# Kernel tuning notes

Hardware: AMD Instinct MI355X
Metric: run time of the kernel (lower is better)

## Reference

```python
import jax, jax.numpy as jnp
import numpy as np

SIG = [1, 1, 1, 1, -1]  # Cl(4,1)
NVEC = 5
GA = 1 << NVEC  # 32


def _build_gp_table():
    # Cayley table for the geometric product on blades indexed by bitmask.
    G = np.zeros((GA, GA, GA), np.float32)
    for a in range(GA):
        for b in range(GA):
            s = 0
            t = a >> 1
            while t:
                s += bin(t & b).count('1')
                t >>= 1
            sign = -1.0 if (s & 1) else 1.0
            common = a & b
            for i in range(NVEC):
                if (common >> i) & 1:
                    sign *= SIG[i]
            G[a, b, a ^ b] = sign
    return G

GP_TABLE = jnp.asarray(_build_gp_table())


def geometric_product(x, y):
    return jnp.einsum('...i,...j,ijk->...k', x, y, GP_TABLE)


def manifold_norm(x):
    # normalize each multivector onto the unit sphere in R^32
    return x / (jnp.linalg.norm(x, axis=-1, keepdims=True) + 1e-6)


def versor_linear(x, W, b):
    # channel mixing shared across multivector components: x [..., in, ga]
    return jnp.einsum('...ig,oi->...og', x, W) + b


def layer_norm2d(x, w, b):
    # LayerNorm over last two dims [D, ga] jointly
    mu = jnp.mean(x, axis=(-2, -1), keepdims=True)
    var = jnp.var(x, axis=(-2, -1), keepdims=True)
    return (x - mu) / jnp.sqrt(var + 1e-5) * w + b


def attention(x, Wq, bq, Wk, bk, Wv, bv, Wo, bo, n_heads):
    B, S, D, G = x.shape
    dh = D // n_heads
    q = versor_linear(x, Wq, bq).reshape(B, S, n_heads, dh, G)
    k = versor_linear(x, Wk, bk).reshape(B, S, n_heads, dh, G)
    v = versor_linear(x, Wv, bv).reshape(B, S, n_heads, dh, G)
    scale = 1.0 / np.sqrt(dh * G).astype(np.float32)
    scores = jnp.einsum('bshdg,bthdg->bhst', q, k) * scale
    probs = jax.nn.softmax(scores, axis=-1)
    o = jnp.einsum('bhst,bthdg->bshdg', probs, v).reshape(B, S, D, G)
    return versor_linear(o, Wo, bo)


N_HEADS = 8


def forward(x, Wq, bq, Wk, bk, Wv, bv, Wo, bo, ln1_w, ln1_b, ln2_w, ln2_b,
            gamma1, gamma2, W1, b1, W2, b2, Wr, br, Wc, bc):
    L = Wq.shape[0]
    for l in range(L):
        h = attention(layer_norm2d(x, ln1_w[l], ln1_b[l]),
                      Wq[l], bq[l], Wk[l], bk[l], Wv[l], bv[l], Wo[l], bo[l], N_HEADS)
        x = manifold_norm(x + gamma1[l] * h)
        m = versor_linear(layer_norm2d(x, ln2_w[l], ln2_b[l]), W1[l], b1[l])
        m = versor_linear(jnp.tanh(m), W2[l], b2[l])
        x = manifold_norm(x + gamma2[l] * m)
    # RecursiveRotorAccumulator: log(S)-step inclusive scan of rotors
    delta = versor_linear(x, Wr, br)
    rot = 0.5 * delta
    rot = rot.at[..., 0].add(1.0)
    rot = manifold_norm(rot)
    S = x.shape[1]
    step = 1
    while step < S:
        left = rot[:, :-step]
        right = rot[:, step:]
        comb = manifold_norm(geometric_product(right, left))
        rot = jnp.concatenate([rot[:, :step], comb], axis=1)
        step *= 2
    pooled = rot[:, -1]  # [B, D, ga]
    logits = pooled.reshape(pooled.shape[0], -1) @ Wc.T + bc
    return logits


def setup_inputs() -> dict:
    key = jax.random.key(0)
    B, S, D, G, L, NC = 8, 256, 64, GA, 4, 1000
    E = 4 * D  # expansion hidden
    ks = jax.random.split(key, 16)
    sd = 0.02
    inp = {
        'x': jax.random.normal(ks[0], (B, S, D, G), jnp.float32),
        'Wq': jax.random.normal(ks[1], (L, D, D), jnp.float32) * sd,
        'bq': jnp.zeros((L, D, G), jnp.float32),
        'Wk': jax.random.normal(ks[2], (L, D, D), jnp.float32) * sd,
        'bk': jnp.zeros((L, D, G), jnp.float32),
        'Wv': jax.random.normal(ks[3], (L, D, D), jnp.float32) * sd,
        'bv': jnp.zeros((L, D, G), jnp.float32),
        'Wo': jax.random.normal(ks[4], (L, D, D), jnp.float32) * sd,
        'bo': jnp.zeros((L, D, G), jnp.float32),
        'ln1_w': jnp.ones((L, D, G), jnp.float32),
        'ln1_b': jnp.zeros((L, D, G), jnp.float32),
        'ln2_w': jnp.ones((L, D, G), jnp.float32),
        'ln2_b': jnp.zeros((L, D, G), jnp.float32),
        'gamma1': 1e-5 * jnp.ones((L, D, G), jnp.float32),
        'gamma2': 1e-5 * jnp.ones((L, D, G), jnp.float32),
        'W1': jax.random.normal(ks[5], (L, E, D), jnp.float32) * sd,
        'b1': jnp.zeros((L, E, G), jnp.float32),
        'W2': jax.random.normal(ks[6], (L, D, E), jnp.float32) * sd,
        'b2': jnp.zeros((L, D, G), jnp.float32),
        'Wr': jax.random.normal(ks[7], (D, D), jnp.float32) * sd,
        'br': jnp.zeros((D, G), jnp.float32),
        'Wc': jax.random.normal(ks[8], (NC, D * G), jnp.float32) * sd,
        'bc': jnp.zeros((NC,), jnp.float32),
    }
    return inp


def reference(x, Wq, bq, Wk, bk, Wv, bv, Wo, bo, ln1_w, ln1_b, ln2_w, ln2_b,
              gamma1, gamma2, W1, b1, W2, b2, Wr, br, Wc, bc):
    return forward(x, Wq, bq, Wk, bk, Wv, bv, Wo, bo, ln1_w, ln1_b, ln2_w, ln2_b,
                   gamma1, gamma2, W1, b1, W2, b2, Wr, br, Wc, bc)
```

## Files before the change

### kernel.cpp

```cpp
#include <hip/hip_runtime.h>
#include <hip/hip_bf16.h>

constexpr int kB  = 8;
constexpr int kS  = 256;
constexpr int kD  = 64;
constexpr int kG  = 32;
constexpr int kE  = 256;
constexpr int kNH = 8;
constexpr int kHD = 256;
constexpr int kDG = kD * kG;
constexpr int kT  = kB * kS;
constexpr int kNC = 1000;

using bf16x8 = __attribute__((ext_vector_type(8))) short;
using f32x4  = __attribute__((ext_vector_type(4))) float;

__device__ __forceinline__ short f2bf(float f) {
    unsigned u = __float_as_uint(f);
    unsigned r = (u + 0x7FFFu + ((u >> 16) & 1u)) >> 16;
    return (short)r;
}

__device__ __forceinline__ float tanh_fast(float x) {
    float a = fabsf(x);
    float e = __expf(-2.f * a);
    float t = (1.f - e) / (1.f + e);
    return copysignf(t, x);
}

__global__ __launch_bounds__(256) void cvtw_kernel(
    const float* __restrict__ Wq, const float* __restrict__ Wk,
    const float* __restrict__ Wv, const float* __restrict__ Wo,
    const float* __restrict__ W1, const float* __restrict__ W2,
    unsigned short* __restrict__ dst) {
    int idx = (blockIdx.x * 256 + threadIdx.x) * 4;
    const float* src; int off;
    if      (idx <  16384) { src = Wq; off = 0; }
    else if (idx <  32768) { src = Wk; off = 16384; }
    else if (idx <  49152) { src = Wv; off = 32768; }
    else if (idx <  65536) { src = Wo; off = 49152; }
    else if (idx < 131072) { src = W1; off = 65536; }
    else                   { src = W2; off = 131072; }
    const float4 v = *(const float4*)(src + (idx - off));
    *(short4*)&dst[idx] = make_short4(f2bf(v.x), f2bf(v.y), f2bf(v.z), f2bf(v.w));
}

__global__ __launch_bounds__(256) void ln_kernel(const float* __restrict__ Xin,
                                                 const float* __restrict__ w,
                                                 const float* __restrict__ b,
                                                 float* __restrict__ A) {
    int t = blockIdx.x, tid = threadIdx.x;
    const float* xp = Xin + (size_t)t * kDG;
    __shared__ float r1[256], r2[256];
    float v[8], s = 0.f, ss = 0.f;
#pragma unroll
    for (int j = 0; j < 8; j++) {
        float x = xp[tid + j * 256];
        v[j] = x; s += x; ss += x * x;
    }
    r1[tid] = s; r2[tid] = ss; __syncthreads();
    for (int o = 128; o > 0; o >>= 1) {
        if (tid < o) { r1[tid] += r1[tid + o]; r2[tid] += r2[tid + o]; }
        __syncthreads();
    }
    float mean = r1[0] * (1.f / kDG);
    float var  = r2[0] * (1.f / kDG) - mean * mean;
    float rstd = rsqrtf(var + 1e-5f);
    float* ao = A + (size_t)t * kDG;
#pragma unroll
    for (int j = 0; j < 8; j++) {
        int jj = tid + j * 256;
        ao[jj] = (v[j] - mean) * rstd * w[jj] + b[jj];
    }
}

__device__ __forceinline__ void epi_res_mn_ln(
    const f32x4 (&acc)[4][2], const float* __restrict__ bias,
    const float* __restrict__ Xin, float* __restrict__ Xout,
    const float* __restrict__ gamma,
    const float* __restrict__ lnw, const float* __restrict__ lnb,
    float* __restrict__ Aout, int tok, int l16, int quad, bool do_ln) {
    const size_t tb = (size_t)tok * kDG;
    float xv[4][2][4];
    float s = 0.f, ss = 0.f;
#pragma unroll
    for (int mt = 0; mt < 4; ++mt)
#pragma unroll
        for (int r = 0; r < 4; ++r) {
            int o = mt * 16 + quad * 4 + r;
            float vv[2]; float sq = 0.f;
#pragma unroll
            for (int nt = 0; nt < 2; ++nt) {
                int g = nt * 16 + l16;
                float h = acc[mt][nt][r] + bias[o * kG + g];
                float v = Xin[tb + o * kG + g] + gamma[o * kG + g] * h;
                vv[nt] = v; sq = fmaf(v, v, sq);
            }
#pragma unroll
            for (int off = 1; off < 16; off <<= 1) sq += __shfl_xor(sq, off, 64);
            float rn = 1.f / (sqrtf(sq) + 1e-6f);
#pragma unroll
            for (int nt = 0; nt < 2; ++nt) {
                int g = nt * 16 + l16;
                float x = vv[nt] * rn;
                xv[mt][nt][r] = x;
                Xout[tb + o * kG + g] = x;
                s += x; ss = fmaf(x, x, ss);
            }
        }
    if (!do_ln) return;
#pragma unroll
    for (int off = 1; off < 64; off <<= 1) {
        s += __shfl_xor(s, off, 64); ss += __shfl_xor(ss, off, 64);
    }
    float mean = s * (1.f / kDG);
    float var  = ss * (1.f / kDG) - mean * mean;
    float rstd = rsqrtf(var + 1e-5f);
#pragma unroll
    for (int mt = 0; mt < 4; ++mt)
#pragma unroll
        for (int nt = 0; nt < 2; ++nt) {
            int g = nt * 16 + l16;
#pragma unroll
            for (int r = 0; r < 4; ++r) {
                int o = mt * 16 + quad * 4 + r;
                Aout[tb + o * kG + g] = (xv[mt][nt][r] - mean) * rstd * lnw[o * kG + g] + lnb[o * kG + g];
            }
        }
}

__global__ __launch_bounds__(256) void vlinT_kernel(const float* __restrict__ X,
                                                    const float* __restrict__ W,
                                                    const float* __restrict__ bias,
                                                    float* __restrict__ OutT) {
    __shared__ float sx[kDG];
    __shared__ float sw[kD * kD];
    int t = blockIdx.x, tid = threadIdx.x;
    const float* xp = X + (size_t)t * kDG;
    for (int j = tid; j < kDG; j += 256) sx[j] = xp[j];
    for (int j = tid; j < kD * kD; j += 256) sw[j] = W[j];
    __syncthreads();
    int g = tid & 31, ob = tid >> 5;
    int b = t >> 8, s = t & 255;
    float* op = OutT + ((size_t)b * kD * kS + s) * kG;
    for (int o = ob; o < kD; o += 8) {
        float acc = bias[o * kG + g];
        const float* wr = sw + o * kD;
#pragma unroll
        for (int i = 0; i < kD; i++) acc += wr[i] * sx[i * kG + g];
        op[(size_t)o * kS * kG + g] = acc;
    }
}

__global__ __launch_bounds__(256, 2) void mlp1_kernel(
    const float* __restrict__ X, const unsigned short* __restrict__ Wh,
    const float* __restrict__ bias, unsigned short* __restrict__ outH) {
    constexpr int M = 256;
    constexpr int WS = 64 + 8;
    __shared__ short sW[M * WS];
    __shared__ short sXT[4][32][WS];

    const int tid = threadIdx.x, wave = tid >> 6, lane = tid & 63;
    const int l16 = lane & 15, quad = lane >> 4;
    const int tok = blockIdx.x * 4 + wave;

    for (int j = tid * 8; j < M * 64; j += 2048) {
        int o = j >> 6, i = j & 63;
        *(bf16x8*)&sW[o * WS + i] = *(const bf16x8*)(Wh + j);
    }
    {
        const int g4 = (lane & 7) * 4;
        const int i0 = (lane >> 3) * 8;
        const float* xp = X + (size_t)tok * kDG;
#pragma unroll
        for (int half = 0; half < 2; ++half) {
            float4 vr[4];
#pragma unroll
            for (int r = 0; r < 4; ++r)
                vr[r] = *(const float4*)(xp + (i0 + half * 4 + r) * kG + g4);
#pragma unroll
            for (int gg = 0; gg < 4; ++gg)
                *(short4*)&sXT[wave][g4 + gg][i0 + half * 4] =
                    make_short4(f2bf((&vr[0].x)[gg]), f2bf((&vr[1].x)[gg]),
                                f2bf((&vr[2].x)[gg]), f2bf((&vr[3].x)[gg]));
        }
    }
    __syncthreads();

    bf16x8 bfr[2][2];
#pragma unroll
    for (int c = 0; c < 2; ++c)
#pragma unroll
        for (int nt = 0; nt < 2; ++nt)
            bfr[c][nt] = *(const bf16x8*)&sXT[wave][nt * 16 + l16][c * 32 + quad * 8];

    f32x4 acc[16][2];
#pragma unroll
    for (int mt = 0; mt < 16; ++mt)
#pragma unroll
        for (int nt = 0; nt < 2; ++nt) acc[mt][nt] = (f32x4){0.f, 0.f, 0.f, 0.f};

#pragma unroll
    for (int mt = 0; mt < 16; ++mt)
#pragma unroll
        for (int c = 0; c < 2; ++c) {
            bf16x8 afr = *(const bf16x8*)&sW[(mt * 16 + l16) * WS + c * 32 + quad * 8];
#pragma unroll
            for (int nt = 0; nt < 2; ++nt)
                acc[mt][nt] = __builtin_amdgcn_mfma_f32_16x16x32_bf16(afr, bfr[c][nt], acc[mt][nt], 0, 0, 0);
        }

    unsigned short* op = outH + (size_t)tok * M * kG;
#pragma unroll
    for (int mt = 0; mt < 16; ++mt)
#pragma unroll
        for (int nt = 0; nt < 2; ++nt) {
            int g = nt * 16 + l16;
            int e0 = mt * 16 + quad * 4;
            short4 s4;
            s4.x = f2bf(tanh_fast(acc[mt][nt][0] + bias[(e0 + 0) * kG + g]));
            s4.y = f2bf(tanh_fast(acc[mt][nt][1] + bias[(e0 + 1) * kG + g]));
            s4.z = f2bf(tanh_fast(acc[mt][nt][2] + bias[(e0 + 2) * kG + g]));
            s4.w = f2bf(tanh_fast(acc[mt][nt][3] + bias[(e0 + 3) * kG + g]));
            *(short4*)&op[g * M + e0] = s4;
        }
}

__global__ __launch_bounds__(256, 3) void gemmWo_fused_kernel(
    const float* __restrict__ X, const unsigned short* __restrict__ Wh,
    const float* __restrict__ bias,
    const float* __restrict__ Xin, const float* __restrict__ gamma,
    const float* __restrict__ lnw, const float* __restrict__ lnb,
    float* __restrict__ Xout, float* __restrict__ Aout) {
    constexpr int WS = 64 + 8;
    __shared__ short sW[64 * WS];
    __shared__ short sXT[4][32][WS];

    const int tid = threadIdx.x, wave = tid >> 6, lane = tid & 63;
    const int l16 = lane & 15, quad = lane >> 4;
    const int tok = blockIdx.x * 4 + wave;

    for (int j = tid * 8; j < 64 * 64; j += 2048) {
        int o = j >> 6, i = j & 63;
        *(bf16x8*)&sW[o * WS + i] = *(const bf16x8*)(Wh + j);
    }
    {
        const int g4 = (lane & 7) * 4;
        const int i0 = (lane >> 3) * 8;
        const float* xp = X + (size_t)tok * kDG;
#pragma unroll
        for (int half = 0; half < 2; ++half) {
            float4 vr[4];
#pragma unroll
            for (int r = 0; r < 4; ++r)
                vr[r] = *(const float4*)(xp + (i0 + half * 4 + r) * kG + g4);
#pragma unroll
            for (int gg = 0; gg < 4; ++gg)
                *(short4*)&sXT[wave][g4 + gg][i0 + half * 4] =
                    make_short4(f2bf((&vr[0].x)[gg]), f2bf((&vr[1].x)[gg]),
                                f2bf((&vr[2].x)[gg]), f2bf((&vr[3].x)[gg]));
        }
    }
    __syncthreads();

    bf16x8 bfr[2][2];
#pragma unroll
    for (int c = 0; c < 2; ++c)
#pragma unroll
        for (int nt = 0; nt < 2; ++nt)
            bfr[c][nt] = *(const bf16x8*)&sXT[wave][nt * 16 + l16][c * 32 + quad * 8];

    f32x4 acc[4][2];
#pragma unroll
    for (int mt = 0; mt < 4; ++mt)
#pragma unroll
        for (int nt = 0; nt < 2; ++nt) acc[mt][nt] = (f32x4){0.f, 0.f, 0.f, 0.f};

#pragma unroll
    for (int mt = 0; mt < 4; ++mt)
#pragma unroll
        for (int c = 0; c < 2; ++c) {
            bf16x8 afr = *(const bf16x8*)&sW[(mt * 16 + l16) * WS + c * 32 + quad * 8];
#pragma unroll
            for (int nt = 0; nt < 2; ++nt)
                acc[mt][nt] = __builtin_amdgcn_mfma_f32_16x16x32_bf16(afr, bfr[c][nt], acc[mt][nt], 0, 0, 0);
        }

    epi_res_mn_ln(acc, bias, Xin, Xout, gamma, lnw, lnb, Aout, tok, l16, quad, true);
}

__global__ __launch_bounds__(256, 3) void gemm_qkv_kernel(
    const float* __restrict__ X,
    const unsigned short* __restrict__ Wqh, const unsigned short* __restrict__ Wkh,
    const unsigned short* __restrict__ Wvh,
    const float* __restrict__ bq, const float* __restrict__ bk, const float* __restrict__ bv,
    unsigned short* __restrict__ Q, unsigned short* __restrict__ K, unsigned short* __restrict__ V) {
    constexpr int WS = 64 + 8;
    __shared__ short sW[3 * 64 * WS];
    __shared__ short sXT[4][32][WS];

    const int tid = threadIdx.x, wave = tid >> 6, lane = tid & 63;
    const int l16 = lane & 15, quad = lane >> 4;
    const int tok = blockIdx.x * 4 + wave;

    const unsigned short* Wp[3] = {Wqh, Wkh, Wvh};
#pragma unroll
    for (int w = 0; w < 3; ++w)
        for (int j = tid * 8; j < 64 * 64; j += 2048) {
            int o = j >> 6, i = j & 63;
            *(bf16x8*)&sW[w * 64 * WS + o * WS + i] = *(const bf16x8*)(Wp[w] + j);
        }
    {
        const int g4 = (lane & 7) * 4;
        const int i0 = (lane >> 3) * 8;
        const float* xp = X + (size_t)tok * kDG;
#pragma unroll
        for (int half = 0; half < 2; ++half) {
            float4 vr[4];
#pragma unroll
            for (int r = 0; r < 4; ++r)
                vr[r] = *(const float4*)(xp + (i0 + half * 4 + r) * kG + g4);
#pragma unroll
            for (int gg = 0; gg < 4; ++gg)
                *(short4*)&sXT[wave][g4 + gg][i0 + half * 4] =
                    make_short4(f2bf((&vr[0].x)[gg]), f2bf((&vr[1].x)[gg]),
                                f2bf((&vr[2].x)[gg]), f2bf((&vr[3].x)[gg]));
        }
    }
    __syncthreads();

    bf16x8 bfr[2][2];
#pragma unroll
    for (int c = 0; c < 2; ++c)
#pragma unroll
        for (int nt = 0; nt < 2; ++nt)
            bfr[c][nt] = *(const bf16x8*)&sXT[wave][nt * 16 + l16][c * 32 + quad * 8];

    f32x4 acc[3][4][2];
#pragma unroll
    for (int w = 0; w < 3; ++w)
#pragma unroll
        for (int mt = 0; mt < 4; ++mt)
#pragma unroll
            for (int nt = 0; nt < 2; ++nt) acc[w][mt][nt] = (f32x4){0.f, 0.f, 0.f, 0.f};

#pragma unroll
    for (int w = 0; w < 3; ++w)
#pragma unroll
        for (int mt = 0; mt < 4; ++mt)
#pragma unroll
            for (int c = 0; c < 2; ++c) {
                bf16x8 afr = *(const bf16x8*)&sW[w * 64 * WS + (mt * 16 + l16) * WS + c * 32 + quad * 8];
#pragma unroll
                for (int nt = 0; nt < 2; ++nt)
                    acc[w][mt][nt] = __builtin_amdgcn_mfma_f32_16x16x32_bf16(afr, bfr[c][nt], acc[w][mt][nt], 0, 0, 0);
            }

    unsigned short* Op[3] = {Q, K, V};
    const float* Bp[3] = {bq, bk, bv};
#pragma unroll
    for (int w = 0; w < 3; ++w) {
        unsigned short* op = Op[w] + (size_t)tok * kDG;
#pragma unroll
        for (int mt = 0; mt < 4; ++mt)
#pragma unroll
            for (int nt = 0; nt < 2; ++nt) {
                int g = nt * 16 + l16;
#pragma unroll
                for (int r = 0; r < 4; ++r) {
                    int o = mt * 16 + quad * 4 + r;
                    op[o * kG + g] = (unsigned short)f2bf(acc[w][mt][nt][r] + Bp[w][o * kG + g]);
                }
            }
    }
}

template<bool DO_LN>
__global__ __launch_bounds__(256, 3) void mlp2_fused_kernel(
    const unsigned short* __restrict__ Mb,
    const unsigned short* __restrict__ W2h, const float* __restrict__ b2,
    float* __restrict__ X, const float* __restrict__ gamma,
    const float* __restrict__ lnw, const float* __restrict__ lnb,
    float* __restrict__ Aout) {
    constexpr int WS = 256 + 8;
    __shared__ short sW[64 * WS];
    const int tid = threadIdx.x, wave = tid >> 6, lane = tid & 63;
    const int l16 = lane & 15, quad = lane >> 4;
    const int tok = blockIdx.x * 4 + wave;

    for (int j = tid * 8; j < 64 * 256; j += 2048) {
        int o = j >> 8, i = j & 255;
        *(bf16x8*)&sW[o * WS + i] = *(const bf16x8*)(W2h + j);
    }
    __syncthreads();

    f32x4 acc[4][2];
#pragma unroll
    for (int mt = 0; mt < 4; ++mt)
#pragma unroll
        for (int nt = 0; nt < 2; ++nt) acc[mt][nt] = (f32x4){0.f, 0.f, 0.f, 0.f};

    const unsigned short* mp = Mb + (size_t)tok * kG * kE;
#pragma unroll
    for (int c = 0; c < 8; ++c) {
        bf16x8 bfr[2];
#pragma unroll
        for (int nt = 0; nt < 2; ++nt)
            bfr[nt] = *(const bf16x8*)&mp[(nt * 16 + l16) * kE + c * 32 + quad * 8];
#pragma unroll
        for (int mt = 0; mt < 4; ++mt) {
            bf16x8 afr = *(const bf16x8*)&sW[(mt * 16 + l16) * WS + c * 32 + quad * 8];
#pragma unroll
            for (int nt = 0; nt < 2; ++nt)
                acc[mt][nt] = __builtin_amdgcn_mfma_f32_16x16x32_bf16(afr, bfr[nt], acc[mt][nt], 0, 0, 0);
        }
    }

    epi_res_mn_ln(acc, b2, X, X, gamma, lnw, lnb, Aout, tok, l16, quad, DO_LN);
}

constexpr int QSTR = 264;
constexpr int VSTR = 40;

__global__ __launch_bounds__(256) void attn_mfma_kernel(const unsigned short* __restrict__ Q,
                                                        const unsigned short* __restrict__ K,
                                                        const unsigned short* __restrict__ V,
                                                        float* __restrict__ O) {
    __shared__ short sQ[64 * QSTR];
    __shared__ short sKV[2][256 * VSTR];

    const int qt = blockIdx.x, h = blockIdx.y, b = blockIdx.z;
    const int tid = threadIdx.x;
    const int wave = tid >> 6, lane = tid & 63;
    const int l16 = lane & 15, quad = lane >> 4;

    const size_t bh = (size_t)b * kS * kDG + (size_t)h * kHD;

#pragma unroll
    for (int it = 0; it < 8; ++it) {
        int j = it * 2048 + tid * 8;
        int row = j >> 8, col = j & 255;
        *(bf16x8*)&sQ[row * QSTR + col] =
            *(const bf16x8*)(Q + bh + (size_t)(qt * 64 + row) * kDG + col);
    }
#pragma unroll
    for (int it = 0; it < 4; ++it) {
        int j = it * 2048 + tid * 8;
        int row = j >> 8, col = j & 255;
        *(bf16x8*)&sKV[0][row * QSTR + col] =
            *(const bf16x8*)(K + bh + (size_t)row * kDG + col);
    }
    __syncthreads();

    bf16x8 afrag[8];
    {
        int row = wave * 16 + l16;
#pragma unroll
        for (int c = 0; c < 8; ++c)
            afrag[c] = *(const bf16x8*)&sQ[row * QSTR + c * 32 + quad * 8];
    }

    f32x4 acc[16];
#pragma unroll
    for (int i = 0; i < 16; ++i) acc[i] = (f32x4){0.f, 0.f, 0.f, 0.f};

    for (int kt = 0; kt < 8; ++kt) {
        bf16x8 kpre[4];
        if (kt < 7) {
#pragma unroll
            for (int it = 0; it < 4; ++it) {
                int j = it * 2048 + tid * 8;
                int row = j >> 8, col = j & 255;
                kpre[it] = *(const bf16x8*)(K + bh + (size_t)((kt + 1) * 32 + row) * kDG + col);
            }
        }
        const short* kb = sKV[kt & 1];
#pragma unroll
        for (int nt = 0; nt < 2; ++nt) {
            int key = nt * 16 + l16;
            f32x4 a = acc[kt * 2 + nt];
#pragma unroll
            for (int c = 0; c < 8; ++c) {
                bf16x8 bfrag = *(const bf16x8*)&kb[key * QSTR + c * 32 + quad * 8];
                a = __builtin_amdgcn_mfma_f32_16x16x32_bf16(afrag[c], bfrag, a, 0, 0, 0);
            }
            acc[kt * 2 + nt] = a;
        }
        if (kt < 7) {
            short* nb = sKV[(kt + 1) & 1];
#pragma unroll
            for (int it = 0; it < 4; ++it) {
                int j = it * 2048 + tid * 8;
                int row = j >> 8, col = j & 255;
                *(bf16x8*)&nb[row * QSTR + col] = kpre[it];
            }
            __syncthreads();
        }
    }

    float inv[4];
#pragma unroll
    for (int r = 0; r < 4; ++r) {
        float m = -1e30f;
#pragma unroll
        for (int t = 0; t < 16; ++t) m = fmaxf(m, acc[t][r]);
#pragma unroll
        for (int off = 1; off < 16; off <<= 1) m = fmaxf(m, __shfl_xor(m, off, 16));
        float s = 0.f;
#pragma unroll
        for (int t = 0; t < 16; ++t) {
            float p = __expf((acc[t][r] - m) * 0.0625f);
            acc[t][r] = p; s += p;
        }
#pragma unroll
        for (int off = 1; off < 16; off <<= 1) s += __shfl_xor(s, off, 16);
        inv[r] = 1.f / s;
    }

#pragma unroll
    for (int t = 0; t < 16; ++t)
#pragma unroll
        for (int r = 0; r < 4; ++r)
            sQ[(wave * 16 + quad * 4 + r) * QSTR + t * 16 + l16] = f2bf(acc[t][r]);

    {
        int kb = tid >> 5;
#pragma unroll
        for (int it = 0; it < 2; ++it) {
            int db = (tid & 31) + it * 32;
            short4 vr[4];
#pragma unroll
            for (int r = 0; r < 4; ++r)
                vr[r] = *(const short4*)(V + bh + (size_t)(kb * 4 + r) * kDG + db * 4);
#pragma unroll
            for (int i = 0; i < 4; ++i) {
                short4 p = make_short4((&vr[0].x)[i], (&vr[1].x)[i],
                                       (&vr[2].x)[i], (&vr[3].x)[i]);
                *(short4*)&sKV[0][(db * 4 + i) * VSTR + kb * 4] = p;
            }
        }
    }
    __syncthreads();

    f32x4 oacc[16];
#pragma unroll
    for (int i = 0; i < 16; ++i) oacc[i] = (f32x4){0.f, 0.f, 0.f, 0.f};

    for (int vt = 0; vt < 8; ++vt) {
        short4 vpre[8];
        if (vt < 7) {
            int kb = tid >> 5;
#pragma unroll
            for (int it = 0; it < 2; ++it) {
                int db = (tid & 31) + it * 32;
#pragma unroll
                for (int r = 0; r < 4; ++r)
                    vpre[it * 4 + r] = *(const short4*)(V + bh + (size_t)((vt + 1) * 32 + kb * 4 + r) * kDG + db * 4);
            }
        }
        const short* vb = sKV[vt & 1];
        bf16x8 pfrag = *(const bf16x8*)&sQ[(wave * 16 + l16) * QSTR + vt * 32 + quad * 8];
#pragma unroll
        for (int dt = 0; dt < 16; ++dt) {
            bf16x8 vfrag = *(const bf16x8*)&vb[(dt * 16 + l16) * VSTR + quad * 8];
            oacc[dt] = __builtin_amdgcn_mfma_f32_16x16x32_bf16(pfrag, vfrag, oacc[dt], 0, 0, 0);
        }
        if (vt < 7) {
            short* nb = sKV[(vt + 1) & 1];
            int kb = tid >> 5;
#pragma unroll
            for (int it = 0; it < 2; ++it) {
                int db = (tid & 31) + it * 32;
#pragma unroll
                for (int i = 0; i < 4; ++i) {
                    short4 p = make_short4((&vpre[it * 4 + 0].x)[i], (&vpre[it * 4 + 1].x)[i],
                                           (&vpre[it * 4 + 2].x)[i], (&vpre[it * 4 + 3].x)[i]);
                    *(short4*)&nb[(db * 4 + i) * VSTR + kb * 4] = p;
                }
            }
            __syncthreads();
        }
    }

    {
        int qrow = qt * 64 + wave * 16 + quad * 4;
#pragma unroll
        for (int dt = 0; dt < 16; ++dt)
#pragma unroll
            for (int r = 0; r < 4; ++r)
                O[bh + (size_t)(qrow + r) * kDG + dt * 16 + l16] = oacc[dt][r] * inv[r];
    }
}

constexpr int pc_ce(unsigned v) { int c = 0; while (v) { c += v & 1; v >>= 1; } return c; }
constexpr unsigned gp_mask_ce(int a) {
    unsigned m = 0;
    for (int c = 0; c < 32; ++c) {
        int b = a ^ c;
        int s = (a & b) >> 4;
        for (int t = a >> 1; t; t >>= 1) s += pc_ce(t & b);
        if (s & 1) m |= (1u << c);
    }
    return m;
}

template<int A>
__device__ __forceinline__ void gp_term(const float* x, const float* y, float* acc) {
    constexpr unsigned m = gp_mask_ce(A);
    const float xa = x[A], nxa = -xa;
#pragma unroll
    for (int c = 0; c < 32; ++c)
        acc[c] = fmaf(((m >> c) & 1u) ? nxa : xa, y[A ^ c], acc[c]);
}

__device__ __forceinline__ void gp_mn_t(const float* x, const float* y, float* out) {
    float acc[32];
#pragma unroll
    for (int c = 0; c < 32; ++c) acc[c] = 0.f;
    gp_term<0>(x, y, acc);  gp_term<1>(x, y, acc);  gp_term<2>(x, y, acc);  gp_term<3>(x, y, acc);
    gp_term<4>(x, y, acc);  gp_term<5>(x, y, acc);  gp_term<6>(x, y, acc);  gp_term<7>(x, y, acc);
    gp_term<8>(x, y, acc);  gp_term<9>(x, y, acc);  gp_term<10>(x, y, acc); gp_term<11>(x, y, acc);
    gp_term<12>(x, y, acc); gp_term<13>(x, y, acc); gp_term<14>(x, y, acc); gp_term<15>(x, y, acc);
    gp_term<16>(x, y, acc); gp_term<17>(x, y, acc); gp_term<18>(x, y, acc); gp_term<19>(x, y, acc);
    gp_term<20>(x, y, acc); gp_term<21>(x, y, acc); gp_term<22>(x, y, acc); gp_term<23>(x, y, acc);
    gp_term<24>(x, y, acc); gp_term<25>(x, y, acc); gp_term<26>(x, y, acc); gp_term<27>(x, y, acc);
    gp_term<28>(x, y, acc); gp_term<29>(x, y, acc); gp_term<30>(x, y, acc); gp_term<31>(x, y, acc);
    float ss = 0.f;
#pragma unroll
    for (int c = 0; c < 32; ++c) ss = fmaf(acc[c], acc[c], ss);
    float r = 1.f / (sqrtf(ss) + 1e-6f);
#pragma unroll
    for (int c = 0; c < 32; ++c) out[c] = acc[c] * r;
}

__device__ __forceinline__ void leaf_load(const float* base, float* v) {
#pragma unroll
    for (int i = 0; i < 8; ++i) {
        const float4 f = *(const float4*)(base + i * 4);
        v[i * 4 + 0] = 0.5f * f.x; v[i * 4 + 1] = 0.5f * f.y;
        v[i * 4 + 2] = 0.5f * f.z; v[i * 4 + 3] = 0.5f * f.w;
    }
    v[0] += 1.f;
    float ss = 0.f;
#pragma unroll
    for (int c = 0; c < 32; ++c) ss = fmaf(v[c], v[c], ss);
    float r = 1.f / (sqrtf(ss) + 1e-6f);
#pragma unroll
    for (int c = 0; c < 32; ++c) v[c] *= r;
}

__global__ __launch_bounds__(256) void scanreg_kernel(const float* __restrict__ DT,
                                                      float* __restrict__ pooled) {
    const int wave = threadIdx.x >> 6, lane = threadIdx.x & 63;
    const int seq = blockIdx.x * 4 + wave;
    const float* base = DT + ((size_t)seq * kS + lane * 4) * kG;

    float R[32], Y[32], P[32], Xa[32], Yb[32];

    leaf_load(base, R);
    for (int j = 1; j < 4; ++j) {
        leaf_load(base + j * kG, Y);
        gp_mn_t(Y, R, R);
    }

    for (int step = 1; step < 64; step <<= 1) {
        const bool up = lane & step;
#pragma unroll
        for (int c = 0; c < 32; ++c) P[c] = __shfl_xor(R[c], step, 64);
#pragma unroll
        for (int c = 0; c < 32; ++c) {
            Xa[c] = up ? R[c] : P[c];
            Yb[c] = up ? P[c] : R[c];
        }
        gp_mn_t(Xa, Yb, R);
    }

    if (lane == 0) {
        float* op = pooled + (size_t)seq * kG;
#pragma unroll
        for (int i = 0; i < 8; ++i)
            *(float4*)(op + i * 4) = make_float4(R[i * 4], R[i * 4 + 1], R[i * 4 + 2], R[i * 4 + 3]);
    }
}

__global__ __launch_bounds__(256) void cls2_kernel(const float* __restrict__ P,
                                                   const float* __restrict__ Wc,
                                                   const float* __restrict__ bc,
                                                   float* __restrict__ out) {
    __shared__ float sp[kB * kDG];
    const int tid = threadIdx.x, wave = tid >> 6, lane = tid & 63;
    for (int j = tid * 4; j < kB * kDG; j += 1024)
        *(float4*)&sp[j] = *(const float4*)(P + j);
    __syncthreads();

    const int c = blockIdx.x * 4 + wave;
    const float* w = Wc + (size_t)c * kDG;
    float acc[kB];
#pragma unroll
    for (int b = 0; b < kB; ++b) acc[b] = 0.f;
#pragma unroll
    for (int cc = 0; cc < 8; ++cc) {
        const float4 w4 = *(const float4*)(w + cc * 256 + lane * 4);
#pragma unroll
        for (int b = 0; b < kB; ++b) {
            const float4 p4 = *(const float4*)&sp[b * kDG + cc * 256 + lane * 4];
            acc[b] += w4.x * p4.x + w4.y * p4.y + w4.z * p4.z + w4.w * p4.w;
        }
    }
#pragma unroll
    for (int b = 0; b < kB; ++b)
#pragma unroll
        for (int off = 32; off > 0; off >>= 1) acc[b] += __shfl_xor(acc[b], off, 64);
    if (lane == 0) {
        float bias = bc[c];
#pragma unroll
        for (int b = 0; b < kB; ++b) out[b * kNC + c] = acc[b] + bias;
    }
}

extern "C" void kernel_launch(void* const* d_in, const int* in_sizes, int n_in,
                              void* d_out, int out_size, void* d_ws, size_t ws_size,
                              hipStream_t stream) {
    const float* x_in = (const float*)d_in[0];
    const float* Wq   = (const float*)d_in[1];
    const float* bq   = (const float*)d_in[2];
    const float* Wk   = (const float*)d_in[3];
    const float* bk   = (const float*)d_in[4];
    const float* Wv   = (const float*)d_in[5];
    const float* bv   = (const float*)d_in[6];
    const float* Wo   = (const float*)d_in[7];
    const float* bo   = (const float*)d_in[8];
    const float* ln1w = (const float*)d_in[9];
    const float* ln1b = (const float*)d_in[10];
    const float* ln2w = (const float*)d_in[11];
    const float* ln2b = (const float*)d_in[12];
    const float* gm1  = (const float*)d_in[13];
    const float* gm2  = (const float*)d_in[14];
    const float* W1   = (const float*)d_in[15];
    const float* b1   = (const float*)d_in[16];
    const float* W2   = (const float*)d_in[17];
    const float* b2   = (const float*)d_in[18];
    const float* Wr   = (const float*)d_in[19];
    const float* br   = (const float*)d_in[20];
    const float* Wc   = (const float*)d_in[21];
    const float* bc   = (const float*)d_in[22];

    const size_t NEL = (size_t)kT * kDG;
    float* F  = (float*)d_ws;
    float* X  = F;
    float* A  = F + NEL;
    unsigned short* Qh = (unsigned short*)(F + 2 * NEL);
    unsigned short* Kh = (unsigned short*)(F + 3 * NEL);
    unsigned short* Vh = (unsigned short*)(F + 4 * NEL);
    unsigned short* Mb = (unsigned short*)(F + 3 * NEL);
    unsigned short* Wb = (unsigned short*)(F + 5 * NEL);
    float* pooled = F + 2 * NEL;
    float* DT = A;

    cvtw_kernel<<<192, 256, 0, stream>>>(Wq, Wk, Wv, Wo, W1, W2, Wb);
    unsigned short* Wqh = Wb;
    unsigned short* Wkh = Wb + 16384;
    unsigned short* Wvh = Wb + 32768;
    unsigned short* Woh = Wb + 49152;
    unsigned short* W1h = Wb + 65536;
    unsigned short* W2h = Wb + 131072;

    ln_kernel<<<kT, 256, 0, stream>>>(x_in, ln1w, ln1b, A);

    for (int l = 0; l < 4; l++) {
        gemm_qkv_kernel<<<kT / 4, 256, 0, stream>>>(A,
            Wqh + l * 4096, Wkh + l * 4096, Wvh + l * 4096,
            bq + l * kDG, bk + l * kDG, bv + l * kDG, Qh, Kh, Vh);
        attn_mfma_kernel<<<dim3(4, kNH, kB), 256, 0, stream>>>(Qh, Kh, Vh, A);
        gemmWo_fused_kernel<<<kT / 4, 256, 0, stream>>>(A, Woh + l * 4096, bo + l * kDG,
            l == 0 ? x_in : X, gm1 + l * kDG, ln2w + l * kDG, ln2b + l * kDG, X, A);
        mlp1_kernel<<<kT / 4, 256, 0, stream>>>(A, W1h + l * 16384, b1 + l * kE * kG, Mb);
        if (l < 3)
            mlp2_fused_kernel<true><<<kT / 4, 256, 0, stream>>>(Mb, W2h + l * 16384, b2 + l * kDG,
                X, gm2 + l * kDG, ln1w + (l + 1) * kDG, ln1b + (l + 1) * kDG, A);
        else
            mlp2_fused_kernel<false><<<kT / 4, 256, 0, stream>>>(Mb, W2h + l * 16384, b2 + l * kDG,
                X, gm2 + l * kDG, nullptr, nullptr, nullptr);
    }

    vlinT_kernel<<<kT, 256, 0, stream>>>(X, Wr, br, DT);
    scanreg_kernel<<<kB * kD / 4, 256, 0, stream>>>(DT, pooled);
    cls2_kernel<<<kNC / 4, 256, 0, stream>>>(pooled, Wc, bc, (float*)d_out);
}
```

Baseline: 544.0 us.

## Store intermediate activations as transposed bf16 to skip per-GEMM conversion staging

The shared activation buffer A becomes bf16 and is stored in a [token][g][channel] transposed layout. It is written this way by the layernorm, attention output and fused epilogues. The consuming GEMM kernels then load MFMA B-fragments straight from global memory, dropping the fp32 load, bf16 convert and LDS transpose stage. This halves activation traffic and removes LDS staging. In exchange, the producers do scattered or transposed stores, and the fp32 precision of these intermediates is lost earlier.

Measured after the change: 571.7 us. 5.1% more time.

```diff
diff --git a/kernel.cpp b/kernel.cpp
--- a/kernel.cpp
+++ b/kernel.cpp
@@ -48,10 +48,11 @@
 __global__ __launch_bounds__(256) void ln_kernel(const float* __restrict__ Xin,
                                                  const float* __restrict__ w,
                                                  const float* __restrict__ b,
-                                                 float* __restrict__ A) {
+                                                 unsigned short* __restrict__ A) {
     int t = blockIdx.x, tid = threadIdx.x;
     const float* xp = Xin + (size_t)t * kDG;
     __shared__ float r1[256], r2[256];
+    __shared__ short st[32 * 72];
     float v[8], s = 0.f, ss = 0.f;
 #pragma unroll
     for (int j = 0; j < 8; j++) {
@@ -66,12 +67,15 @@
     float mean = r1[0] * (1.f / kDG);
     float var  = r2[0] * (1.f / kDG) - mean * mean;
     float rstd = rsqrtf(var + 1e-5f);
-    float* ao = A + (size_t)t * kDG;
 #pragma unroll
     for (int j = 0; j < 8; j++) {
         int jj = tid + j * 256;
-        ao[jj] = (v[j] - mean) * rstd * w[jj] + b[jj];
-    }
+        float val = (v[j] - mean) * rstd * w[jj] + b[jj];
+        st[(jj & 31) * 72 + (jj >> 5)] = f2bf(val);
+    }
+    __syncthreads();
+    bf16x8 ov = *(const bf16x8*)&st[(tid >> 3) * 72 + (tid & 7) * 8];
+    *(bf16x8*)&A[(size_t)t * kDG + tid * 8] = ov;
 }
 
 __device__ __forceinline__ void epi_res_mn_ln(
@@ -79,7 +83,7 @@
     const float* __restrict__ Xin, float* __restrict__ Xout,
     const float* __restrict__ gamma,
     const float* __restrict__ lnw, const float* __restrict__ lnb,
-    float* __restrict__ Aout, int tok, int l16, int quad, bool do_ln) {
+    unsigned short* __restrict__ Aout, int tok, int l16, int quad, bool do_ln) {
     const size_t tb = (size_t)tok * kDG;
     float xv[4][2][4];
     float s = 0.f, ss = 0.f;
@@ -116,16 +120,21 @@
     float mean = s * (1.f / kDG);
     float var  = ss * (1.f / kDG) - mean * mean;
     float rstd = rsqrtf(var + 1e-5f);
+    unsigned short* aop = Aout + tb;
 #pragma unroll
     for (int mt = 0; mt < 4; ++mt)
 #pragma unroll
         for (int nt = 0; nt < 2; ++nt) {
             int g = nt * 16 + l16;
+            int o0 = mt * 16 + quad * 4;
+            short4 s4;
 #pragma unroll
             for (int r = 0; r < 4; ++r) {
-                int o = mt * 16 + quad * 4 + r;
-                Aout[tb + o * kG + g] = (xv[mt][nt][r] - mean) * rstd * lnw[o * kG + g] + lnb[o * kG + g];
-            }
+                int o = o0 + r;
+                float lv = (xv[mt][nt][r] - mean) * rstd * lnw[o * kG + g] + lnb[o * kG + g];
+                (&s4.x)[r] = f2bf(lv);
+            }
+            *(short4*)&aop[g * kD + o0] = s4;
         }
 }
 
@@ -153,12 +162,11 @@
 }
 
 __global__ __launch_bounds__(256, 2) void mlp1_kernel(
-    const float* __restrict__ X, const unsigned short* __restrict__ Wh,
+    const unsigned short* __restrict__ X, const unsigned short* __restrict__ Wh,
     const float* __restrict__ bias, unsigned short* __restrict__ outH) {
     constexpr int M = 256;
     constexpr int WS = 64 + 8;
     __shared__ short sW[M * WS];
-    __shared__ short sXT[4][32][WS];
 
     const int tid = threadIdx.x, wave = tid >> 6, lane = tid & 63;
     const int l16 = lane & 15, quad = lane >> 4;
@@ -168,31 +176,15 @@
         int o = j >> 6, i = j & 63;
         *(bf16x8*)&sW[o * WS + i] = *(const bf16x8*)(Wh + j);
     }
-    {
-        const int g4 = (lane & 7) * 4;
-        const int i0 = (lane >> 3) * 8;
-        const float* xp = X + (size_t)tok * kDG;
-#pragma unroll
-        for (int half = 0; half < 2; ++half) {
-            float4 vr[4];
-#pragma unroll
-            for (int r = 0; r < 4; ++r)
-                vr[r] = *(const float4*)(xp + (i0 + half * 4 + r) * kG + g4);
-#pragma unroll
-            for (int gg = 0; gg < 4; ++gg)
-                *(short4*)&sXT[wave][g4 + gg][i0 + half * 4] =
-                    make_short4(f2bf((&vr[0].x)[gg]), f2bf((&vr[1].x)[gg]),
-                                f2bf((&vr[2].x)[gg]), f2bf((&vr[3].x)[gg]));
-        }
-    }
-    __syncthreads();
-
+
+    const unsigned short* xp = X + (size_t)tok * kDG;
     bf16x8 bfr[2][2];
 #pragma unroll
     for (int c = 0; c < 2; ++c)
 #pragma unroll
         for (int nt = 0; nt < 2; ++nt)
-            bfr[c][nt] = *(const bf16x8*)&sXT[wave][nt * 16 + l16][c * 32 + quad * 8];
+            bfr[c][nt] = *(const bf16x8*)&xp[(nt * 16 + l16) * kD + c * 32 + quad * 8];
+    __syncthreads();
 
     f32x4 acc[16][2];
 #pragma unroll
@@ -227,14 +219,13 @@
 }
 
 __global__ __launch_bounds__(256, 3) void gemmWo_fused_kernel(
-    const float* __restrict__ X, const unsigned short* __restrict__ Wh,
+    const unsigned short* __restrict__ X, const unsigned short* __restrict__ Wh,
     const float* __restrict__ bias,
     const float* __restrict__ Xin, const float* __restrict__ gamma,
     const float* __restrict__ lnw, const float* __restrict__ lnb,
-    float* __restrict__ Xout, float* __restrict__ Aout) {
+    float* __restrict__ Xout, unsigned short* __restrict__ Aout) {
     constexpr int WS = 64 + 8;
     __shared__ short sW[64 * WS];
-    __shared__ short sXT[4][32][WS];
 
     const int tid = threadIdx.x, wave = tid >> 6, lane = tid & 63;
     const int l16 = lane & 15, quad = lane >> 4;
@@ -244,31 +235,15 @@
         int o = j >> 6, i = j & 63;
         *(bf16x8*)&sW[o * WS + i] = *(const bf16x8*)(Wh + j);
     }
-    {
-        const int g4 = (lane & 7) * 4;
-        const int i0 = (lane >> 3) * 8;
-        const float* xp = X + (size_t)tok * kDG;
-#pragma unroll
-        for (int half = 0; half < 2; ++half) {
-            float4 vr[4];
-#pragma unroll
-            for (int r = 0; r < 4; ++r)
-                vr[r] = *(const float4*)(xp + (i0 + half * 4 + r) * kG + g4);
-#pragma unroll
-            for (int gg = 0; gg < 4; ++gg)
-                *(short4*)&sXT[wave][g4 + gg][i0 + half * 4] =
-                    make_short4(f2bf((&vr[0].x)[gg]), f2bf((&vr[1].x)[gg]),
-                                f2bf((&vr[2].x)[gg]), f2bf((&vr[3].x)[gg]));
-        }
-    }
-    __syncthreads();
-
+
+    const unsigned short* xp = X + (size_t)tok * kDG;
     bf16x8 bfr[2][2];
 #pragma unroll
     for (int c = 0; c < 2; ++c)
 #pragma unroll
         for (int nt = 0; nt < 2; ++nt)
-            bfr[c][nt] = *(const bf16x8*)&sXT[wave][nt * 16 + l16][c * 32 + quad * 8];
+            bfr[c][nt] = *(const bf16x8*)&xp[(nt * 16 + l16) * kD + c * 32 + quad * 8];
+    __syncthreads();
 
     f32x4 acc[4][2];
 #pragma unroll
@@ -290,14 +265,13 @@
 }
 
 __global__ __launch_bounds__(256, 3) void gemm_qkv_kernel(
-    const float* __restrict__ X,
+    const unsigned short* __restrict__ X,
     const unsigned short* __restrict__ Wqh, const unsigned short* __restrict__ Wkh,
     const unsigned short* __restrict__ Wvh,
     const float* __restrict__ bq, const float* __restrict__ bk, const float* __restrict__ bv,
     unsigned short* __restrict__ Q, unsigned short* __restrict__ K, unsigned short* __restrict__ V) {
     constexpr int WS = 64 + 8;
     __shared__ short sW[3 * 64 * WS];
-    __shared__ short sXT[4][32][WS];
 
     const int tid = threadIdx.x, wave = tid >> 6, lane = tid & 63;
     const int l16 = lane & 15, quad = lane >> 4;
@@ -310,31 +284,15 @@
             int o = j >> 6, i = j & 63;
             *(bf16x8*)&sW[w * 64 * WS + o * WS + i] = *(const bf16x8*)(Wp[w] + j);
         }
-    {
-        const int g4 = (lane & 7) * 4;
-        const int i0 = (lane >> 3) * 8;
-        const float* xp = X + (size_t)tok * kDG;
-#pragma unroll
-        for (int half = 0; half < 2; ++half) {
-            float4 vr[4];
-#pragma unroll
-            for (int r = 0; r < 4; ++r)
-                vr[r] = *(const float4*)(xp + (i0 + half * 4 + r) * kG + g4);
-#pragma unroll
-            for (int gg = 0; gg < 4; ++gg)
-                *(short4*)&sXT[wave][g4 + gg][i0 + half * 4] =
-                    make_short4(f2bf((&vr[0].x)[gg]), f2bf((&vr[1].x)[gg]),
-                                f2bf((&vr[2].x)[gg]), f2bf((&vr[3].x)[gg]));
-        }
-    }
-    __syncthreads();
-
+
+    const unsigned short* xp = X + (size_t)tok * kDG;
     bf16x8 bfr[2][2];
 #pragma unroll
     for (int c = 0; c < 2; ++c)
 #pragma unroll
         for (int nt = 0; nt < 2; ++nt)
-            bfr[c][nt] = *(const bf16x8*)&sXT[wave][nt * 16 + l16][c * 32 + quad * 8];
+            bfr[c][nt] = *(const bf16x8*)&xp[(nt * 16 + l16) * kD + c * 32 + quad * 8];
+    __syncthreads();
 
     f32x4 acc[3][4][2];
 #pragma unroll
@@ -381,7 +339,7 @@
     const unsigned short* __restrict__ W2h, const float* __restrict__ b2,
     float* __restrict__ X, const float* __restrict__ gamma,
     const float* __restrict__ lnw, const float* __restrict__ lnb,
-    float* __restrict__ Aout) {
+    unsigned short* __restrict__ Aout) {
     constexpr int WS = 256 + 8;
     __shared__ short sW[64 * WS];
     const int tid = threadIdx.x, wave = tid >> 6, lane = tid & 63;
@@ -425,7 +383,7 @@
 __global__ __launch_bounds__(256) void attn_mfma_kernel(const unsigned short* __restrict__ Q,
                                                         const unsigned short* __restrict__ K,
                                                         const unsigned short* __restrict__ V,
-                                                        float* __restrict__ O) {
+                                                        unsigned short* __restrict__ O) {
     __shared__ short sQ[64 * QSTR];
     __shared__ short sKV[2][256 * VSTR];
 
@@ -583,12 +541,19 @@
     }
 
     {
-        int qrow = qt * 64 + wave * 16 + quad * 4;
-#pragma unroll
-        for (int dt = 0; dt < 16; ++dt)
-#pragma unroll
-            for (int r = 0; r < 4; ++r)
-                O[bh + (size_t)(qrow + r) * kDG + dt * 16 + l16] = oacc[dt][r] * inv[r];
+        const size_t ob = (size_t)(b * kS + qt * 64 + wave * 16 + quad * 4) * kDG + h * 8;
+#pragma unroll
+        for (int gg = 0; gg < 2; ++gg) {
+            int g = gg * 16 + l16;
+#pragma unroll
+            for (int r = 0; r < 4; ++r) {
+                bf16x8 pk;
+#pragma unroll
+                for (int k = 0; k < 8; ++k)
+                    pk[k] = f2bf(oacc[k * 2 + gg][r] * inv[r]);
+                *(bf16x8*)&O[ob + (size_t)r * kDG + g * kD] = pk;
+            }
+        }
     }
 }
 
@@ -748,14 +713,14 @@
     const size_t NEL = (size_t)kT * kDG;
     float* F  = (float*)d_ws;
     float* X  = F;
-    float* A  = F + NEL;
+    unsigned short* Abf = (unsigned short*)(F + NEL);
     unsigned short* Qh = (unsigned short*)(F + 2 * NEL);
     unsigned short* Kh = (unsigned short*)(F + 3 * NEL);
     unsigned short* Vh = (unsigned short*)(F + 4 * NEL);
     unsigned short* Mb = (unsigned short*)(F + 3 * NEL);
     unsigned short* Wb = (unsigned short*)(F + 5 * NEL);
     float* pooled = F + 2 * NEL;
-    float* DT = A;
+    float* DT = F + NEL;
 
     cvtw_kernel<<<192, 256, 0, stream>>>(Wq, Wk, Wv, Wo, W1, W2, Wb);
     unsigned short* Wqh = Wb;
@@ -765,19 +730,19 @@
     unsigned short* W1h = Wb + 65536;
     unsigned short* W2h = Wb + 131072;
 
-    ln_kernel<<<kT, 256, 0, stream>>>(x_in, ln1w, ln1b, A);
+    ln_kernel<<<kT, 256, 0, stream>>>(x_in, ln1w, ln1b, Abf);
 
     for (int l = 0; l < 4; l++) {
-        gemm_qkv_kernel<<<kT / 4, 256, 0, stream>>>(A,
+        gemm_qkv_kernel<<<kT / 4, 256, 0, stream>>>(Abf,
             Wqh + l * 4096, Wkh + l * 4096, Wvh + l * 4096,
             bq + l * kDG, bk + l * kDG, bv + l * kDG, Qh, Kh, Vh);
-        attn_mfma_kernel<<<dim3(4, kNH, kB), 256, 0, stream>>>(Qh, Kh, Vh, A);
-        gemmWo_fused_kernel<<<kT / 4, 256, 0, stream>>>(A, Woh + l * 4096, bo + l * kDG,
-            l == 0 ? x_in : X, gm1 + l * kDG, ln2w + l * kDG, ln2b + l * kDG, X, A);
-        mlp1_kernel<<<kT / 4, 256, 0, stream>>>(A, W1h + l * 16384, b1 + l * kE * kG, Mb);
+        attn_mfma_kernel<<<dim3(4, kNH, kB), 256, 0, stream>>>(Qh, Kh, Vh, Abf);
+        gemmWo_fused_kernel<<<kT / 4, 256, 0, stream>>>(Abf, Woh + l * 4096, bo + l * kDG,
+            l == 0 ? x_in : X, gm1 + l * kDG, ln2w + l * kDG, ln2b + l * kDG, X, Abf);
+        mlp1_kernel<<<kT / 4, 256, 0, stream>>>(Abf, W1h + l * 16384, b1 + l * kE * kG, Mb);
         if (l < 3)
             mlp2_fused_kernel<true><<<kT / 4, 256, 0, stream>>>(Mb, W2h + l * 16384, b2 + l * kDG,
-                X, gm2 + l * kDG, ln1w + (l + 1) * kDG, ln1b + (l + 1) * kDG, A);
+                X, gm2 + l * kDG, ln1w + (l + 1) * kDG, ln1b + (l + 1) * kDG, Abf);
         else
             mlp2_fused_kernel<false><<<kT / 4, 256, 0, stream>>>(Mb, W2h + l * 16384, b2 + l * kDG,
                 X, gm2 + l * kDG, nullptr, nullptr, nullptr);
```
